# Optimization experiments

Hardware: AMD Instinct MI355X
Metric: run time of the kernel (lower is better)

## Reference

```python
import jax, jax.numpy as jnp
import numpy as np

D_MODEL = 768
NHEAD = 12
WINDOW = 128
FREQ = 10000.0


def _rope(x, freq=FREQ):
    # x: (b, h, l, d). Rotate-half style rotary embedding.
    b, h, l, d = x.shape
    inv_freq = 1.0 / (freq ** (jnp.arange(0, d, 2, dtype=jnp.float32) / d))  # (d/2,)
    ang = jnp.arange(l, dtype=jnp.float32)[:, None] * inv_freq[None, :]      # (l, d/2)
    cos = jnp.cos(ang)[None, None]  # (1,1,l,d/2)
    sin = jnp.sin(ang)[None, None]
    x1, x2 = x[..., : d // 2], x[..., d // 2 :]
    return jnp.concatenate([x1 * cos - x2 * sin, x1 * sin + x2 * cos], axis=-1)


def setup_inputs() -> dict:
    key = jax.random.key(0)
    k0, k1, k2 = jax.random.split(key, 3)
    B, L = 1, 2048
    emb = jax.random.normal(k0, (B, L, D_MODEL), dtype=jnp.float32)
    mask = jnp.ones((B, L), dtype=jnp.int32)
    W_qkv = jax.random.normal(k1, (D_MODEL, 3 * D_MODEL), dtype=jnp.float32) * 0.02
    b_qkv = jnp.zeros((3 * D_MODEL,), dtype=jnp.float32)
    W_o = jax.random.normal(k2, (D_MODEL, D_MODEL), dtype=jnp.float32) * 0.02
    b_o = jnp.zeros((D_MODEL,), dtype=jnp.float32)
    return {"embeddings": emb, "attention_mask": mask, "W_qkv": W_qkv, "b_qkv": b_qkv, "W_o": W_o, "b_o": b_o}


def reference(embeddings, attention_mask, W_qkv, b_qkv, W_o, b_o):
    B, L, D = embeddings.shape
    H, W = NHEAD, WINDOW
    hd = D // H
    scale = 1.0 / jnp.sqrt(jnp.float32(D))  # original divides by d_model**0.5

    qkv = embeddings @ W_qkv + b_qkv                      # (b,l,3D)
    q, k, v = jnp.split(qkv, 3, axis=-1)

    def sep(x):  # (b,l,D) -> (b,h,l,hd)
        return x.reshape(B, L, H, hd).transpose(0, 2, 1, 3)

    q, k, v = sep(q), sep(k), sep(v)
    q = _rope(q)
    k = _rope(k)

    # window indices: centered window of width W, clamped to [0, L-1]
    raw = jnp.arange(L)[:, None] + jnp.arange(W)[None, :] - W // 2  # (L,W)
    idxs = jnp.clip(raw, 0, L - 1)
    in_range = (raw >= 0) & (raw < L)                                # (L,W)

    k_w = k[:, :, idxs, :]  # (b,h,l,w,hd) gathered keys
    v_w = v[:, :, idxs, :]

    scores = jnp.einsum("bhlwd,bhld->bhlw", k_w, q) * scale
    amask = attention_mask.astype(bool)                              # (b,l)
    wmask = amask[:, idxs] & in_range[None]                          # (b,l,w)
    scores = jnp.where(wmask[:, None], scores, -jnp.inf)
    weights = jax.nn.softmax(scores, axis=-1)
    out = jnp.einsum("bhlw,bhlwd->bhld", weights, v_w)               # (b,h,l,hd)

    # CLS global attention (query at position 0 attends to all keys)
    cls_scores = jnp.einsum("bhd,bhld->bhl", q[:, :, 0, :], k) * scale
    cls_scores = jnp.where(amask[:, None], cls_scores, -jnp.inf)
    cls_w = jax.nn.softmax(cls_scores, axis=-1)
    cls_out = jnp.einsum("bhl,bhld->bhd", cls_w, v)                  # (b,h,hd)
    out = out.at[:, :, 0, :].set(cls_out)

    joined = out.transpose(0, 2, 1, 3).reshape(B, L, D)              # join heads
    return joined @ W_o + b_o
```

## Files before the change

### kernel.cpp

```cpp
#include <hip/hip_runtime.h>
#include <hip/hip_bf16.h>
#include <cmath>

#define D_MODEL 768
#define NHEAD 12
#define HD 64
#define L_SEQ 2048
#define WIN 128
#define QKV_N (3 * D_MODEL)

typedef _Float16 half8 __attribute__((ext_vector_type(8)));
typedef _Float16 half4v __attribute__((ext_vector_type(4)));
typedef float floatx4 __attribute__((ext_vector_type(4)));

#define CVT_A_BLKS 1536
#define CVT_B_BLKS (36 * 12)
#define CVT_C_BLKS (12 * 12)

__global__ __launch_bounds__(256) void cvt_fused_kernel(
    const float* __restrict__ emb, _Float16* __restrict__ A16,
    const float* __restrict__ W_qkv, _Float16* __restrict__ Wq16T,
    const float* __restrict__ W_o, _Float16* __restrict__ Wo16T) {
  __shared__ float tile[64][68];
  const int bid = blockIdx.x;
  const int tid = threadIdx.x;

  if (bid < CVT_A_BLKS) {
    const int i = (bid * 256 + tid) * 4;
    const float4 v = *reinterpret_cast<const float4*>(&emb[i]);
    half4v h = {(_Float16)v.x, (_Float16)v.y, (_Float16)v.z, (_Float16)v.w};
    *reinterpret_cast<half4v*>(&A16[i]) = h;
    return;
  }
  const float* In;
  _Float16* Out;
  int R, Cn, bx, by;
  if (bid < CVT_A_BLKS + CVT_B_BLKS) {
    const int b = bid - CVT_A_BLKS;
    In = W_qkv; Out = Wq16T; R = D_MODEL; Cn = QKV_N;
    bx = b % 36; by = b / 36;
  } else {
    const int b = bid - CVT_A_BLKS - CVT_B_BLKS;
    In = W_o; Out = Wo16T; R = D_MODEL; Cn = D_MODEL;
    bx = b % 12; by = b / 12;
  }
  const int r0 = by * 64, c0 = bx * 64;
  const int tr = tid >> 4, tc4 = (tid & 15) * 4;
#pragma unroll
  for (int rr = 0; rr < 4; ++rr) {
    const int r = rr * 16 + tr;
    const float4 v =
        *reinterpret_cast<const float4*>(&In[(size_t)(r0 + r) * Cn + c0 + tc4]);
    tile[r][tc4 + 0] = v.x;
    tile[r][tc4 + 1] = v.y;
    tile[r][tc4 + 2] = v.z;
    tile[r][tc4 + 3] = v.w;
  }
  __syncthreads();
#pragma unroll
  for (int cc = 0; cc < 4; ++cc) {
    const int c = cc * 16 + tr;
    half4v h = {(_Float16)tile[tc4 + 0][c], (_Float16)tile[tc4 + 1][c],
                (_Float16)tile[tc4 + 2][c], (_Float16)tile[tc4 + 3][c]};
    *reinterpret_cast<half4v*>(&Out[(size_t)(c0 + c) * R + r0 + tc4]) = h;
  }
}

template <int BM, int BN, typename OutT, bool ROPE>
__global__ __launch_bounds__(256) void gemm16_kernel(
    const _Float16* __restrict__ A, const _Float16* __restrict__ BT,
    const float* __restrict__ bias, OutT* __restrict__ C,
    _Float16* __restrict__ q16, _Float16* __restrict__ k16,
    _Float16* __restrict__ v16, _Float16* __restrict__ v16T, int M, int N,
    int K) {
  constexpr int LDK = 40;
  constexpr int MF = BM / 32;
  constexpr int NF = BN / 32;
  constexpr int CA = BM * 4 / 256;
  constexpr int CB = BN * 4 / 256;

  __shared__ __align__(16) _Float16 At[BM * LDK];
  __shared__ __align__(16) _Float16 Bt[BN * LDK];

  const int tid = threadIdx.x;
  const int row0 = blockIdx.y * BM;
  const int col0 = blockIdx.x * BN;
  const int wv = tid >> 6;
  const int lane = tid & 63;
  const int wr = wv >> 1;
  const int wc = wv & 1;
  const int lrow = lane & 15;
  const int lk = lane >> 4;

  floatx4 acc[MF][NF];
#pragma unroll
  for (int m = 0; m < MF; ++m)
#pragma unroll
    for (int n = 0; n < NF; ++n) acc[m][n] = (floatx4){0.f, 0.f, 0.f, 0.f};

  half8 aR[CA], bR[CB];
  const int nt = K / 32;

#pragma unroll
  for (int i = 0; i < CA; ++i) {
    const int c = tid + i * 256, r = c >> 2, seg = c & 3;
    aR[i] = *reinterpret_cast<const half8*>(&A[(size_t)(row0 + r) * K + seg * 8]);
  }
#pragma unroll
  for (int i = 0; i < CB; ++i) {
    const int c = tid + i * 256, r = c >> 2, seg = c & 3;
    bR[i] =
        *reinterpret_cast<const half8*>(&BT[(size_t)(col0 + r) * K + seg * 8]);
  }

  for (int t = 0; t < nt; ++t) {
    if (t) __syncthreads();
#pragma unroll
    for (int i = 0; i < CA; ++i) {
      const int c = tid + i * 256, r = c >> 2, seg = c & 3;
      *reinterpret_cast<half8*>(&At[r * LDK + seg * 8]) = aR[i];
    }
#pragma unroll
    for (int i = 0; i < CB; ++i) {
      const int c = tid + i * 256, r = c >> 2, seg = c & 3;
      *reinterpret_cast<half8*>(&Bt[r * LDK + seg * 8]) = bR[i];
    }
    __syncthreads();

    if (t + 1 < nt) {
      const int k0 = (t + 1) * 32;
#pragma unroll
      for (int i = 0; i < CA; ++i) {
        const int c = tid + i * 256, r = c >> 2, seg = c & 3;
        aR[i] = *reinterpret_cast<const half8*>(
            &A[(size_t)(row0 + r) * K + k0 + seg * 8]);
      }
#pragma unroll
      for (int i = 0; i < CB; ++i) {
        const int c = tid + i * 256, r = c >> 2, seg = c & 3;
        bR[i] = *reinterpret_cast<const half8*>(
            &BT[(size_t)(col0 + r) * K + k0 + seg * 8]);
      }
    }

    half8 af[MF], bf[NF];
#pragma unroll
    for (int m = 0; m < MF; ++m)
      af[m] = *reinterpret_cast<const half8*>(
          &At[(wr * (BM / 2) + m * 16 + lrow) * LDK + lk * 8]);
#pragma unroll
    for (int n = 0; n < NF; ++n)
      bf[n] = *reinterpret_cast<const half8*>(
          &Bt[(wc * (BN / 2) + n * 16 + lrow) * LDK + lk * 8]);
#pragma unroll
    for (int m = 0; m < MF; ++m)
#pragma unroll
      for (int n = 0; n < NF; ++n)
        acc[m][n] = __builtin_amdgcn_mfma_f32_16x16x32_f16(af[m], bf[n],
                                                           acc[m][n], 0, 0, 0);
  }

  if constexpr (!ROPE) {
#pragma unroll
    for (int m = 0; m < MF; ++m)
#pragma unroll
      for (int n = 0; n < NF; ++n) {
        const int col = col0 + wc * (BN / 2) + n * 16 + lrow;
        const float bb = bias[col];
#pragma unroll
        for (int j = 0; j < 4; ++j) {
          const int row = row0 + wr * (BM / 2) + m * 16 + lk * 4 + j;
          C[(size_t)row * N + col] = (OutT)(acc[m][n][j] + bb);
        }
      }
  } else {
    const int part = col0 / D_MODEL;
    const int h = ((col0 % D_MODEL) >> 6) + wc;
    _Float16* dst = (part == 0) ? q16 : (part == 1) ? k16 : v16;
    float bb[4];
#pragma unroll
    for (int n = 0; n < 4; ++n) bb[n] = bias[col0 + wc * 64 + n * 16 + lrow];
    const float inv0 = exp2f(-0.4152410118609203f * (float)lrow);
    const float inv1 = inv0 * 0.01f;
#pragma unroll
    for (int m = 0; m < MF; ++m) {
#pragma unroll
      for (int j = 0; j < 4; ++j) {
        const int l = row0 + wr * (BM / 2) + m * 16 + lk * 4 + j;
        float val[4];
#pragma unroll
        for (int n = 0; n < 4; ++n) val[n] = acc[m][n][j] + bb[n];
        float o[4];
        if (part < 2) {
          float sn0, cs0, sn1, cs1;
          __sincosf((float)l * inv0, &sn0, &cs0);
          __sincosf((float)l * inv1, &sn1, &cs1);
          o[0] = val[0] * cs0 - val[2] * sn0;
          o[1] = val[1] * cs1 - val[3] * sn1;
          o[2] = val[0] * sn0 + val[2] * cs0;
          o[3] = val[1] * sn1 + val[3] * cs1;
        } else {
          o[0] = val[0]; o[1] = val[1]; o[2] = val[2]; o[3] = val[3];
        }
        const size_t base = ((size_t)h * L_SEQ + l) * HD + lrow;
#pragma unroll
        for (int n = 0; n < 4; ++n) dst[base + n * 16] = (_Float16)o[n];
      }
      if (part == 2) {
        const int lb = row0 + wr * (BM / 2) + m * 16 + lk * 4;
#pragma unroll
        for (int n = 0; n < 4; ++n) {
          const int col = h * HD + n * 16 + lrow;
          half4v hv = {(_Float16)(acc[m][n][0] + bb[n]),
                       (_Float16)(acc[m][n][1] + bb[n]),
                       (_Float16)(acc[m][n][2] + bb[n]),
                       (_Float16)(acc[m][n][3] + bb[n])};
          *reinterpret_cast<half4v*>(&v16T[(size_t)col * L_SEQ + lb]) = hv;
        }
      }
    }
  }
}

#define TL 32
#define SLOTS 160
#define LDH 72
#define LDS_S 168
#define LDVT 168
#define CSPLIT 32
#define CROWS (L_SEQ / CSPLIT)
#define CREC 66

__global__ __launch_bounds__(256) void attn_mega_kernel(
    const _Float16* __restrict__ q16, const _Float16* __restrict__ k16,
    const _Float16* __restrict__ v16, const _Float16* __restrict__ v16T,
    const int* __restrict__ mask, _Float16* __restrict__ joined,
    float* __restrict__ part) {
  const int h = blockIdx.y;
  const int tid = threadIdx.x;
  const float scale = 0.036084391824351615f;

  __shared__ __align__(16) _Float16 kv16[SLOTS * LDH];
  __shared__ __align__(16) float sS[TL * LDS_S];
  __shared__ __align__(16) _Float16 q16l[TL * LDH];
  __shared__ float vbias[SLOTS];

  if (blockIdx.x < (L_SEQ / TL)) {
    const int l0 = blockIdx.x * TL;
    const _Float16* kh = k16 + (size_t)h * L_SEQ * HD;
    const _Float16* qh = q16 + (size_t)h * L_SEQ * HD;

    {
      const int row = tid >> 3, oct = (tid & 7) * 8;
      *reinterpret_cast<half8*>(&q16l[row * LDH + oct]) =
          *reinterpret_cast<const half8*>(&qh[(size_t)(l0 + row) * HD + oct]);
    }
    const _Float16* kwin = kh + (size_t)(l0 - WIN / 2) * HD;
#pragma unroll
    for (int c = tid; c < SLOTS * 8; c += 256) {
      const int slot = c >> 3, oct = (c & 7) * 8;
      *reinterpret_cast<half8*>(&kv16[slot * LDH + oct]) =
          *reinterpret_cast<const half8*>(&kwin[(size_t)slot * HD + oct]);
    }
    if (tid < SLOTS) {
      const int raw = l0 + tid - WIN / 2;
      const int idx = min(max(raw, 0), L_SEQ - 1);
      vbias[tid] =
          ((raw >= 0) && (raw < L_SEQ) && (mask[idx] != 0)) ? 0.f : -INFINITY;
    }
    __syncthreads();

    const int wv = tid >> 6, lane = tid & 63;
    const int wr = wv >> 1, wc = wv & 1;
    const int lcol = lane & 15, loct = (lane >> 4) * 8;

    floatx4 accS[5];
#pragma unroll
    for (int f = 0; f < 5; ++f) accS[f] = (floatx4){0.f, 0.f, 0.f, 0.f};
#pragma unroll
    for (int ks = 0; ks < 2; ++ks) {
      const half8 af = *reinterpret_cast<const half8*>(
          &q16l[(wr * 16 + lcol) * LDH + ks * 32 + loct]);
#pragma unroll
      for (int f = 0; f < 5; ++f) {
        const half8 bf = *reinterpret_cast<const half8*>(
            &kv16[(wc * 80 + f * 16 + lcol) * LDH + ks * 32 + loct]);
        accS[f] =
            __builtin_amdgcn_mfma_f32_16x16x32_f16(af, bf, accS[f], 0, 0, 0);
      }
    }
#pragma unroll
    for (int f = 0; f < 5; ++f) {
      const int slot = wc * 80 + f * 16 + lcol;
      const float vb = vbias[slot];
#pragma unroll
      for (int j = 0; j < 4; ++j) {
        const int row = wr * 16 + (lane >> 4) * 4 + j;
        const bool inband = (slot >= row) && (slot <= row + WIN - 1);
        sS[row * LDS_S + slot] = inband ? (accS[f][j] * scale + vb) : -INFINITY;
      }
    }
    __syncthreads();

    _Float16* vt = kv16;
    const _Float16* vtg =
        v16T + (size_t)h * HD * L_SEQ + (l0 - WIN / 2);
#pragma unroll
    for (int c = tid; c < HD * 20; c += 256) {
      const int d = c / 20, seg = c % 20;
      *reinterpret_cast<half8*>(&vt[d * LDVT + seg * 8]) =
          *reinterpret_cast<const half8*>(&vtg[(size_t)d * L_SEQ + seg * 8]);
    }

    const int r = tid >> 3, wg = tid & 7;
    float pv[20];
    float mloc = -INFINITY;
#pragma unroll
    for (int i = 0; i < 20; ++i) {
      pv[i] = sS[r * LDS_S + wg * 20 + i];
      mloc = fmaxf(mloc, pv[i]);
    }
#pragma unroll
    for (int m = 1; m < 8; m <<= 1) mloc = fmaxf(mloc, __shfl_xor(mloc, m));
    float ssum = 0.f;
#pragma unroll
    for (int i = 0; i < 20; ++i) {
      pv[i] = __expf(pv[i] - mloc);
      ssum += pv[i];
    }
#pragma unroll
    for (int m = 1; m < 8; m <<= 1) ssum += __shfl_xor(ssum, m);
    const float rcp = 1.0f / ssum;
    __syncthreads();

    _Float16* pS = reinterpret_cast<_Float16*>(sS);
#pragma unroll
    for (int i = 0; i < 20; ++i)
      pS[r * (2 * LDS_S) + wg * 20 + i] = (_Float16)(pv[i] * rcp);
    __syncthreads();

    floatx4 accO[2];
    accO[0] = (floatx4){0.f, 0.f, 0.f, 0.f};
    accO[1] = (floatx4){0.f, 0.f, 0.f, 0.f};
#pragma unroll
    for (int ks = 0; ks < 5; ++ks) {
      const half8 ap = *reinterpret_cast<const half8*>(
          &pS[(wr * 16 + lcol) * (2 * LDS_S) + ks * 32 + loct]);
#pragma unroll
      for (int cf = 0; cf < 2; ++cf) {
        const half8 bv = *reinterpret_cast<const half8*>(
            &vt[(wc * 32 + cf * 16 + lcol) * LDVT + ks * 32 + loct]);
        accO[cf] =
            __builtin_amdgcn_mfma_f32_16x16x32_f16(ap, bv, accO[cf], 0, 0, 0);
      }
    }
#pragma unroll
    for (int cf = 0; cf < 2; ++cf)
#pragma unroll
      for (int j = 0; j < 4; ++j) {
        const int row = wr * 16 + (lane >> 4) * 4 + j;
        const int d = wc * 32 + cf * 16 + lcol;
        joined[(size_t)(l0 + row) * D_MODEL + h * HD + d] =
            (_Float16)accO[cf][j];
      }
  } else {
    const int sp = blockIdx.x - (L_SEQ / TL);
    const int l0 = sp * CROWS;
    float* scS = sS;
    float* red = sS + CROWS;
    float* pvS = sS + CROWS + 256;

    const _Float16* kh = k16 + (size_t)h * L_SEQ * HD;
    const _Float16* vh = v16 + (size_t)h * L_SEQ * HD;

    const int lq = tid >> 4;
    const int dq = tid & 15;
    const half4v q4 =
        *reinterpret_cast<const half4v*>(&q16[(size_t)h * L_SEQ * HD + dq * 4]);
#pragma unroll
    for (int it = 0; it < CROWS / 16; ++it) {
      const int l = l0 + it * 16 + lq;
      const half4v k4 =
          *reinterpret_cast<const half4v*>(&kh[(size_t)l * HD + dq * 4]);
      float p = (float)q4[0] * (float)k4[0] + (float)q4[1] * (float)k4[1] +
                (float)q4[2] * (float)k4[2] + (float)q4[3] * (float)k4[3];
#pragma unroll
      for (int m = 1; m < 16; m <<= 1) p += __shfl_xor(p, m);
      if (dq == 0) scS[it * 16 + lq] = (mask[l] != 0) ? p * scale : -INFINITY;
    }
    __syncthreads();

    red[tid] = (tid < CROWS) ? scS[tid] : -INFINITY;
    __syncthreads();
    for (int off = 128; off > 0; off >>= 1) {
      if (tid < off) red[tid] = fmaxf(red[tid], red[tid + off]);
      __syncthreads();
    }
    const float mx = red[0];
    __syncthreads();

    float e = 0.f;
    if (tid < CROWS) {
      e = (mx == -INFINITY) ? 0.f : __expf(scS[tid] - mx);
      scS[tid] = e;
    }
    red[tid] = e;
    __syncthreads();
    for (int off = 128; off > 0; off >>= 1) {
      if (tid < off) red[tid] += red[tid + off];
      __syncthreads();
    }
    const float lsum = red[0];
    __syncthreads();

    const int lg = tid >> 6;
    const int d = tid & 63;
    float acc = 0.f;
#pragma unroll 8
    for (int it = 0; it < CROWS / 4; ++it) {
      const int ll = lg + it * 4;
      acc += scS[ll] * (float)vh[(size_t)(l0 + ll) * HD + d];
    }
    pvS[lg * HD + d] = acc;
    __syncthreads();

    float* rec = &part[(size_t)(h * CSPLIT + sp) * CREC];
    if (tid == 0) {
      rec[0] = mx;
      rec[1] = lsum;
    }
    if (tid < HD)
      rec[2 + tid] =
          pvS[0 * HD + tid] + pvS[1 * HD + tid] + pvS[2 * HD + tid] +
          pvS[3 * HD + tid];
  }
}

__global__ __launch_bounds__(64) void cls_combine_kernel(
    const float* __restrict__ part, _Float16* __restrict__ joined) {
  const int h = blockIdx.x;
  const int d = threadIdx.x;

  float gmax = -INFINITY;
#pragma unroll
  for (int sp = 0; sp < CSPLIT; ++sp)
    gmax = fmaxf(gmax, part[(size_t)(h * CSPLIT + sp) * CREC]);

  float total = 0.f, acc = 0.f;
#pragma unroll
  for (int sp = 0; sp < CSPLIT; ++sp) {
    const float* rec = &part[(size_t)(h * CSPLIT + sp) * CREC];
    const float mxi = rec[0];
    const float w = (mxi == -INFINITY) ? 0.f : __expf(mxi - gmax);
    total += w * rec[1];
    acc += w * rec[2 + d];
  }
  joined[(size_t)h * HD + d] = (_Float16)(acc / total);
}

extern "C" void kernel_launch(void* const* d_in, const int* in_sizes, int n_in,
                              void* d_out, int out_size, void* d_ws,
                              size_t ws_size, hipStream_t stream) {
  const float* emb   = (const float*)d_in[0];
  const int*   mask  = (const int*)d_in[1];
  const float* W_qkv = (const float*)d_in[2];
  const float* b_qkv = (const float*)d_in[3];
  const float* W_o   = (const float*)d_in[4];
  const float* b_o   = (const float*)d_in[5];
  float* out = (float*)d_out;

  _Float16* hp = (_Float16*)d_ws;
  _Float16* A16   = hp;
  _Float16* Wq16T = A16 + (size_t)L_SEQ * D_MODEL;
  _Float16* Wo16T = Wq16T + (size_t)QKV_N * D_MODEL;
  _Float16* q16   = Wo16T + (size_t)D_MODEL * D_MODEL;
  _Float16* k16   = q16 + (size_t)NHEAD * L_SEQ * HD;
  _Float16* v16   = k16 + (size_t)NHEAD * L_SEQ * HD;
  _Float16* v16T  = v16 + (size_t)NHEAD * L_SEQ * HD;
  _Float16* J16   = v16T + (size_t)D_MODEL * L_SEQ;
  float*    part  = (float*)(J16 + (size_t)L_SEQ * D_MODEL);

  cvt_fused_kernel<<<CVT_A_BLKS + CVT_B_BLKS + CVT_C_BLKS, 256, 0, stream>>>(
      emb, A16, W_qkv, Wq16T, W_o, Wo16T);

  gemm16_kernel<64, 128, _Float16, true>
      <<<dim3(QKV_N / 128, L_SEQ / 64), 256, 0, stream>>>(
          A16, Wq16T, b_qkv, (_Float16*)nullptr, q16, k16, v16, v16T, L_SEQ,
          QKV_N, D_MODEL);

  attn_mega_kernel<<<dim3(L_SEQ / TL + CSPLIT, NHEAD), 256, 0, stream>>>(
      q16, k16, v16, v16T, mask, J16, part);

  cls_combine_kernel<<<NHEAD, 64, 0, stream>>>(part, J16);

  gemm16_kernel<64, 64, float, false>
      <<<dim3(D_MODEL / 64, L_SEQ / 64), 256, 0, stream>>>(
          J16, Wo16T, b_o, out, (_Float16*)nullptr, (_Float16*)nullptr,
          (_Float16*)nullptr, (_Float16*)nullptr, L_SEQ, D_MODEL, D_MODEL);
}
```

Before: 123.8 us.

## Fuse embedding fp16 conversion into QKV GEMM, CLS combine into output GEMM, double-buffer LDS

The QKV GEMM now reads fp32 embeddings directly and converts them to fp16 in registers, which removes the separate conversion pass and its intermediate buffer. The CLS combine step is folded into the output-projection GEMM: the row-0 blocks compute the combined CLS vector into LDS and use it as row 0 of A, so one kernel launch is dropped. The GEMM main loop also moves to double-buffered LDS with one barrier per K step. In exchange, the QKV GEMM reads twice the A bytes, the row-0 blocks do serial combine work before their GEMM starts, and LDS use doubles.

Measured after the change: 144.0 us. 16.3% more time.

```diff
diff --git a/kernel.cpp b/kernel.cpp
--- a/kernel.cpp
+++ b/kernel.cpp
@@ -13,34 +13,24 @@
 typedef _Float16 half4v __attribute__((ext_vector_type(4)));
 typedef float floatx4 __attribute__((ext_vector_type(4)));
 
-#define CVT_A_BLKS 1536
 #define CVT_B_BLKS (36 * 12)
 #define CVT_C_BLKS (12 * 12)
 
 __global__ __launch_bounds__(256) void cvt_fused_kernel(
-    const float* __restrict__ emb, _Float16* __restrict__ A16,
     const float* __restrict__ W_qkv, _Float16* __restrict__ Wq16T,
     const float* __restrict__ W_o, _Float16* __restrict__ Wo16T) {
   __shared__ float tile[64][68];
   const int bid = blockIdx.x;
   const int tid = threadIdx.x;
 
-  if (bid < CVT_A_BLKS) {
-    const int i = (bid * 256 + tid) * 4;
-    const float4 v = *reinterpret_cast<const float4*>(&emb[i]);
-    half4v h = {(_Float16)v.x, (_Float16)v.y, (_Float16)v.z, (_Float16)v.w};
-    *reinterpret_cast<half4v*>(&A16[i]) = h;
-    return;
-  }
   const float* In;
   _Float16* Out;
   int R, Cn, bx, by;
-  if (bid < CVT_A_BLKS + CVT_B_BLKS) {
-    const int b = bid - CVT_A_BLKS;
+  if (bid < CVT_B_BLKS) {
     In = W_qkv; Out = Wq16T; R = D_MODEL; Cn = QKV_N;
-    bx = b % 36; by = b / 36;
+    bx = bid % 36; by = bid / 36;
   } else {
-    const int b = bid - CVT_A_BLKS - CVT_B_BLKS;
+    const int b = bid - CVT_B_BLKS;
     In = W_o; Out = Wo16T; R = D_MODEL; Cn = D_MODEL;
     bx = b % 12; by = b / 12;
   }
@@ -66,12 +56,16 @@
   }
 }
 
-template <int BM, int BN, typename OutT, bool ROPE>
+#define CSPLIT 32
+#define CREC 66
+
+template <int BM, int BN, typename OutT, bool ROPE, bool A32, bool COMBINE>
 __global__ __launch_bounds__(256) void gemm16_kernel(
-    const _Float16* __restrict__ A, const _Float16* __restrict__ BT,
-    const float* __restrict__ bias, OutT* __restrict__ C,
-    _Float16* __restrict__ q16, _Float16* __restrict__ k16,
-    _Float16* __restrict__ v16, _Float16* __restrict__ v16T, int M, int N,
+    const float* __restrict__ Af, const _Float16* __restrict__ Ah,
+    const _Float16* __restrict__ BT, const float* __restrict__ bias,
+    OutT* __restrict__ C, _Float16* __restrict__ q16,
+    _Float16* __restrict__ k16, _Float16* __restrict__ v16,
+    _Float16* __restrict__ v16T, const float* __restrict__ part, int M, int N,
     int K) {
   constexpr int LDK = 40;
   constexpr int MF = BM / 32;
@@ -79,8 +73,9 @@
   constexpr int CA = BM * 4 / 256;
   constexpr int CB = BN * 4 / 256;
 
-  __shared__ __align__(16) _Float16 At[BM * LDK];
-  __shared__ __align__(16) _Float16 Bt[BN * LDK];
+  __shared__ __align__(16) _Float16 At[2 * BM * LDK];
+  __shared__ __align__(16) _Float16 Bt[2 * BN * LDK];
+  __shared__ __align__(16) _Float16 comb[COMBINE ? D_MODEL : 1];
 
   const int tid = threadIdx.x;
   const int row0 = blockIdx.y * BM;
@@ -91,6 +86,32 @@
   const int wc = wv & 1;
   const int lrow = lane & 15;
   const int lk = lane >> 4;
+  const bool doComb = COMBINE && (blockIdx.y == 0);
+
+  if constexpr (COMBINE) {
+    if (doComb) {
+#pragma unroll
+      for (int j = 0; j < D_MODEL / 256; ++j) {
+        const int c = tid + j * 256;
+        const int h = c >> 6, d = c & 63;
+        float gmax = -INFINITY;
+#pragma unroll 8
+        for (int sp = 0; sp < CSPLIT; ++sp)
+          gmax = fmaxf(gmax, part[(size_t)(h * CSPLIT + sp) * CREC]);
+        float total = 0.f, acc = 0.f;
+#pragma unroll 8
+        for (int sp = 0; sp < CSPLIT; ++sp) {
+          const float* rec = &part[(size_t)(h * CSPLIT + sp) * CREC];
+          const float mxi = rec[0];
+          const float w = (mxi == -INFINITY) ? 0.f : __expf(mxi - gmax);
+          total += w * rec[1];
+          acc += w * rec[2 + d];
+        }
+        comb[c] = (_Float16)(acc / total);
+      }
+      __syncthreads();
+    }
+  }
 
   floatx4 acc[MF][NF];
 #pragma unroll
@@ -101,63 +122,77 @@
   half8 aR[CA], bR[CB];
   const int nt = K / 32;
 
-#pragma unroll
-  for (int i = 0; i < CA; ++i) {
-    const int c = tid + i * 256, r = c >> 2, seg = c & 3;
-    aR[i] = *reinterpret_cast<const half8*>(&A[(size_t)(row0 + r) * K + seg * 8]);
-  }
-#pragma unroll
-  for (int i = 0; i < CB; ++i) {
-    const int c = tid + i * 256, r = c >> 2, seg = c & 3;
-    bR[i] =
-        *reinterpret_cast<const half8*>(&BT[(size_t)(col0 + r) * K + seg * 8]);
-  }
-
-  for (int t = 0; t < nt; ++t) {
-    if (t) __syncthreads();
+  auto load_regs = [&](int t) {
+    const int k0 = t * 32;
 #pragma unroll
     for (int i = 0; i < CA; ++i) {
       const int c = tid + i * 256, r = c >> 2, seg = c & 3;
-      *reinterpret_cast<half8*>(&At[r * LDK + seg * 8]) = aR[i];
+      if constexpr (A32) {
+        const float4 f0 = *reinterpret_cast<const float4*>(
+            &Af[(size_t)(row0 + r) * K + k0 + seg * 8]);
+        const float4 f1 = *reinterpret_cast<const float4*>(
+            &Af[(size_t)(row0 + r) * K + k0 + seg * 8 + 4]);
+        aR[i] = (half8){(_Float16)f0.x, (_Float16)f0.y, (_Float16)f0.z,
+                        (_Float16)f0.w, (_Float16)f1.x, (_Float16)f1.y,
+                        (_Float16)f1.z, (_Float16)f1.w};
+      } else {
+        if (COMBINE && doComb && r == 0) {
+          aR[i] = *reinterpret_cast<const half8*>(&comb[k0 + seg * 8]);
+        } else {
+          aR[i] = *reinterpret_cast<const half8*>(
+              &Ah[(size_t)(row0 + r) * K + k0 + seg * 8]);
+        }
+      }
     }
 #pragma unroll
     for (int i = 0; i < CB; ++i) {
       const int c = tid + i * 256, r = c >> 2, seg = c & 3;
-      *reinterpret_cast<half8*>(&Bt[r * LDK + seg * 8]) = bR[i];
-    }
-    __syncthreads();
-
-    if (t + 1 < nt) {
-      const int k0 = (t + 1) * 32;
-#pragma unroll
-      for (int i = 0; i < CA; ++i) {
-        const int c = tid + i * 256, r = c >> 2, seg = c & 3;
-        aR[i] = *reinterpret_cast<const half8*>(
-            &A[(size_t)(row0 + r) * K + k0 + seg * 8]);
-      }
-#pragma unroll
-      for (int i = 0; i < CB; ++i) {
-        const int c = tid + i * 256, r = c >> 2, seg = c & 3;
-        bR[i] = *reinterpret_cast<const half8*>(
-            &BT[(size_t)(col0 + r) * K + k0 + seg * 8]);
-      }
-    }
-
+      bR[i] = *reinterpret_cast<const half8*>(
+          &BT[(size_t)(col0 + r) * K + k0 + seg * 8]);
+    }
+  };
+  auto store_lds = [&](int buf) {
+    _Float16* a = &At[buf * BM * LDK];
+    _Float16* b = &Bt[buf * BN * LDK];
+#pragma unroll
+    for (int i = 0; i < CA; ++i) {
+      const int c = tid + i * 256, r = c >> 2, seg = c & 3;
+      *reinterpret_cast<half8*>(&a[r * LDK + seg * 8]) = aR[i];
+    }
+#pragma unroll
+    for (int i = 0; i < CB; ++i) {
+      const int c = tid + i * 256, r = c >> 2, seg = c & 3;
+      *reinterpret_cast<half8*>(&b[r * LDK + seg * 8]) = bR[i];
+    }
+  };
+
+  load_regs(0);
+  store_lds(0);
+  int cur = 0;
+
+  for (int t = 0; t < nt; ++t) {
+    __syncthreads();
+    if (t + 1 < nt) load_regs(t + 1);
+
+    const _Float16* a = &At[cur * BM * LDK];
+    const _Float16* b = &Bt[cur * BN * LDK];
     half8 af[MF], bf[NF];
 #pragma unroll
     for (int m = 0; m < MF; ++m)
       af[m] = *reinterpret_cast<const half8*>(
-          &At[(wr * (BM / 2) + m * 16 + lrow) * LDK + lk * 8]);
+          &a[(wr * (BM / 2) + m * 16 + lrow) * LDK + lk * 8]);
 #pragma unroll
     for (int n = 0; n < NF; ++n)
       bf[n] = *reinterpret_cast<const half8*>(
-          &Bt[(wc * (BN / 2) + n * 16 + lrow) * LDK + lk * 8]);
+          &b[(wc * (BN / 2) + n * 16 + lrow) * LDK + lk * 8]);
 #pragma unroll
     for (int m = 0; m < MF; ++m)
 #pragma unroll
       for (int n = 0; n < NF; ++n)
         acc[m][n] = __builtin_amdgcn_mfma_f32_16x16x32_f16(af[m], bf[n],
                                                            acc[m][n], 0, 0, 0);
+    if (t + 1 < nt) store_lds(cur ^ 1);
+    cur ^= 1;
   }
 
   if constexpr (!ROPE) {
@@ -174,9 +209,9 @@
         }
       }
   } else {
-    const int part = col0 / D_MODEL;
+    const int part_id = col0 / D_MODEL;
     const int h = ((col0 % D_MODEL) >> 6) + wc;
-    _Float16* dst = (part == 0) ? q16 : (part == 1) ? k16 : v16;
+    _Float16* dst = (part_id == 0) ? q16 : (part_id == 1) ? k16 : v16;
     float bb[4];
 #pragma unroll
     for (int n = 0; n < 4; ++n) bb[n] = bias[col0 + wc * 64 + n * 16 + lrow];
@@ -191,7 +226,7 @@
 #pragma unroll
         for (int n = 0; n < 4; ++n) val[n] = acc[m][n][j] + bb[n];
         float o[4];
-        if (part < 2) {
+        if (part_id < 2) {
           float sn0, cs0, sn1, cs1;
           __sincosf((float)l * inv0, &sn0, &cs0);
           __sincosf((float)l * inv1, &sn1, &cs1);
@@ -206,7 +241,7 @@
 #pragma unroll
         for (int n = 0; n < 4; ++n) dst[base + n * 16] = (_Float16)o[n];
       }
-      if (part == 2) {
+      if (part_id == 2) {
         const int lb = row0 + wr * (BM / 2) + m * 16 + lk * 4;
 #pragma unroll
         for (int n = 0; n < 4; ++n) {
@@ -227,9 +262,7 @@
 #define LDH 72
 #define LDS_S 168
 #define LDVT 168
-#define CSPLIT 32
 #define CROWS (L_SEQ / CSPLIT)
-#define CREC 66
 
 __global__ __launch_bounds__(256) void attn_mega_kernel(
     const _Float16* __restrict__ q16, const _Float16* __restrict__ k16,
@@ -303,8 +336,7 @@
     __syncthreads();
 
     _Float16* vt = kv16;
-    const _Float16* vtg =
-        v16T + (size_t)h * HD * L_SEQ + (l0 - WIN / 2);
+    const _Float16* vtg = v16T + (size_t)h * HD * L_SEQ + (l0 - WIN / 2);
 #pragma unroll
     for (int c = tid; c < HD * 20; c += 256) {
       const int d = c / 20, seg = c % 20;
@@ -430,32 +462,9 @@
       rec[1] = lsum;
     }
     if (tid < HD)
-      rec[2 + tid] =
-          pvS[0 * HD + tid] + pvS[1 * HD + tid] + pvS[2 * HD + tid] +
-          pvS[3 * HD + tid];
-  }
-}
-
-__global__ __launch_bounds__(64) void cls_combine_kernel(
-    const float* __restrict__ part, _Float16* __restrict__ joined) {
-  const int h = blockIdx.x;
-  const int d = threadIdx.x;
-
-  float gmax = -INFINITY;
-#pragma unroll
-  for (int sp = 0; sp < CSPLIT; ++sp)
-    gmax = fmaxf(gmax, part[(size_t)(h * CSPLIT + sp) * CREC]);
-
-  float total = 0.f, acc = 0.f;
-#pragma unroll
-  for (int sp = 0; sp < CSPLIT; ++sp) {
-    const float* rec = &part[(size_t)(h * CSPLIT + sp) * CREC];
-    const float mxi = rec[0];
-    const float w = (mxi == -INFINITY) ? 0.f : __expf(mxi - gmax);
-    total += w * rec[1];
-    acc += w * rec[2 + d];
-  }
-  joined[(size_t)h * HD + d] = (_Float16)(acc / total);
+      rec[2 + tid] = pvS[0 * HD + tid] + pvS[1 * HD + tid] +
+                     pvS[2 * HD + tid] + pvS[3 * HD + tid];
+  }
 }
 
 extern "C" void kernel_launch(void* const* d_in, const int* in_sizes, int n_in,
@@ -470,8 +479,7 @@
   float* out = (float*)d_out;
 
   _Float16* hp = (_Float16*)d_ws;
-  _Float16* A16   = hp;
-  _Float16* Wq16T = A16 + (size_t)L_SEQ * D_MODEL;
+  _Float16* Wq16T = hp;
   _Float16* Wo16T = Wq16T + (size_t)QKV_N * D_MODEL;
   _Float16* q16   = Wo16T + (size_t)D_MODEL * D_MODEL;
   _Float16* k16   = q16 + (size_t)NHEAD * L_SEQ * HD;
@@ -480,21 +488,20 @@
   _Float16* J16   = v16T + (size_t)D_MODEL * L_SEQ;
   float*    part  = (float*)(J16 + (size_t)L_SEQ * D_MODEL);
 
-  cvt_fused_kernel<<<CVT_A_BLKS + CVT_B_BLKS + CVT_C_BLKS, 256, 0, stream>>>(
-      emb, A16, W_qkv, Wq16T, W_o, Wo16T);
-
-  gemm16_kernel<64, 128, _Float16, true>
+  cvt_fused_kernel<<<CVT_B_BLKS + CVT_C_BLKS, 256, 0, stream>>>(
+      W_qkv, Wq16T, W_o, Wo16T);
+
+  gemm16_kernel<64, 128, _Float16, true, true, false>
       <<<dim3(QKV_N / 128, L_SEQ / 64), 256, 0, stream>>>(
-          A16, Wq16T, b_qkv, (_Float16*)nullptr, q16, k16, v16, v16T, L_SEQ,
-          QKV_N, D_MODEL);
+          emb, (const _Float16*)nullptr, Wq16T, b_qkv, (_Float16*)nullptr, q16,
+          k16, v16, v16T, (const float*)nullptr, L_SEQ, QKV_N, D_MODEL);
 
   attn_mega_kernel<<<dim3(L_SEQ / TL + CSPLIT, NHEAD), 256, 0, stream>>>(
       q16, k16, v16, v16T, mask, J16, part);
 
-  cls_combine_kernel<<<NHEAD, 64, 0, stream>>>(part, J16);
-
-  gemm16_kernel<64, 64, float, false>
+  gemm16_kernel<64, 64, float, false, false, true>
       <<<dim3(D_MODEL / 64, L_SEQ / 64), 256, 0, stream>>>(
-          J16, Wo16T, b_o, out, (_Float16*)nullptr, (_Float16*)nullptr,
-          (_Float16*)nullptr, (_Float16*)nullptr, L_SEQ, D_MODEL, D_MODEL);
+          (const float*)nullptr, J16, Wo16T, b_o, out, (_Float16*)nullptr,
+          (_Float16*)nullptr, (_Float16*)nullptr, (_Float16*)nullptr, part,
+          L_SEQ, D_MODEL, D_MODEL);
 }
```

## Double-buffer GEMM tiles with direct global-to-LDS async copies and XOR swizzle

Applied to the files above, without the earlier changes.

Replaces the register-staged GEMM tile loading with `global_load_lds` direct-to-shared copies into two ping-pong LDS buffers. This removes the register round trip and leaves one barrier per K step instead of two. The padded LDS layout is replaced by an XOR swizzle on 16-byte segments to avoid bank conflicts. The risk is that correctness relies on the barrier waiting for outstanding vector-memory loads and on the swizzle mapping matching between writer and reader lanes.

Result: no change. 125.0 us (+1.0%).

```diff
diff --git a/kernel.cpp b/kernel.cpp
--- a/kernel.cpp
+++ b/kernel.cpp
@@ -12,6 +12,11 @@
 typedef _Float16 half8 __attribute__((ext_vector_type(8)));
 typedef _Float16 half4v __attribute__((ext_vector_type(4)));
 typedef float floatx4 __attribute__((ext_vector_type(4)));
+
+#define ASYNC_COPY16(gptr, lptr)                                      \
+  __builtin_amdgcn_global_load_lds(                                   \
+      (const __attribute__((address_space(1))) void*)(gptr),          \
+      (__attribute__((address_space(3))) void*)(lptr), 16, 0, 0)
 
 #define CVT_A_BLKS 1536
 #define CVT_B_BLKS (36 * 12)
@@ -73,14 +78,13 @@
     _Float16* __restrict__ q16, _Float16* __restrict__ k16,
     _Float16* __restrict__ v16, _Float16* __restrict__ v16T, int M, int N,
     int K) {
-  constexpr int LDK = 40;
+  static_assert(BM == 64, "staging assignment assumes BM==64");
   constexpr int MF = BM / 32;
   constexpr int NF = BN / 32;
-  constexpr int CA = BM * 4 / 256;
-  constexpr int CB = BN * 4 / 256;
-
-  __shared__ __align__(16) _Float16 At[BM * LDK];
-  __shared__ __align__(16) _Float16 Bt[BN * LDK];
+  constexpr int NBPW = BN / 64;
+
+  __shared__ __align__(16) _Float16 At[2 * BM * 32];
+  __shared__ __align__(16) _Float16 Bt[2 * BN * 32];
 
   const int tid = threadIdx.x;
   const int row0 = blockIdx.y * BM;
@@ -92,72 +96,58 @@
   const int lrow = lane & 15;
   const int lk = lane >> 4;
 
+  const int segg = (((lane & 3) ^ ((lane >> 2) & 3) ^ (lane >> 4)) << 3);
+
+  const _Float16* gA =
+      A + (size_t)(row0 + wv * 16 + (lane >> 2)) * K + segg;
+  const _Float16* gB[NBPW];
+#pragma unroll
+  for (int i = 0; i < NBPW; ++i)
+    gB[i] = BT + (size_t)(col0 + (wv + 4 * i) * 16 + (lane >> 2)) * K + segg;
+
   floatx4 acc[MF][NF];
 #pragma unroll
   for (int m = 0; m < MF; ++m)
 #pragma unroll
     for (int n = 0; n < NF; ++n) acc[m][n] = (floatx4){0.f, 0.f, 0.f, 0.f};
 
-  half8 aR[CA], bR[CB];
   const int nt = K / 32;
 
-#pragma unroll
-  for (int i = 0; i < CA; ++i) {
-    const int c = tid + i * 256, r = c >> 2, seg = c & 3;
-    aR[i] = *reinterpret_cast<const half8*>(&A[(size_t)(row0 + r) * K + seg * 8]);
-  }
-#pragma unroll
-  for (int i = 0; i < CB; ++i) {
-    const int c = tid + i * 256, r = c >> 2, seg = c & 3;
-    bR[i] =
-        *reinterpret_cast<const half8*>(&BT[(size_t)(col0 + r) * K + seg * 8]);
-  }
-
+  ASYNC_COPY16(gA, &At[wv * 512]);
+#pragma unroll
+  for (int i = 0; i < NBPW; ++i)
+    ASYNC_COPY16(gB[i], &Bt[(wv + 4 * i) * 512]);
+
+  int cur = 0;
   for (int t = 0; t < nt; ++t) {
-    if (t) __syncthreads();
-#pragma unroll
-    for (int i = 0; i < CA; ++i) {
-      const int c = tid + i * 256, r = c >> 2, seg = c & 3;
-      *reinterpret_cast<half8*>(&At[r * LDK + seg * 8]) = aR[i];
-    }
-#pragma unroll
-    for (int i = 0; i < CB; ++i) {
-      const int c = tid + i * 256, r = c >> 2, seg = c & 3;
-      *reinterpret_cast<half8*>(&Bt[r * LDK + seg * 8]) = bR[i];
-    }
-    __syncthreads();
-
+    __syncthreads();
     if (t + 1 < nt) {
-      const int k0 = (t + 1) * 32;
-#pragma unroll
-      for (int i = 0; i < CA; ++i) {
-        const int c = tid + i * 256, r = c >> 2, seg = c & 3;
-        aR[i] = *reinterpret_cast<const half8*>(
-            &A[(size_t)(row0 + r) * K + k0 + seg * 8]);
-      }
-#pragma unroll
-      for (int i = 0; i < CB; ++i) {
-        const int c = tid + i * 256, r = c >> 2, seg = c & 3;
-        bR[i] = *reinterpret_cast<const half8*>(
-            &BT[(size_t)(col0 + r) * K + k0 + seg * 8]);
-      }
-    }
-
+      const int ko = (t + 1) * 32;
+      ASYNC_COPY16(gA + ko, &At[(cur ^ 1) * (BM * 32) + wv * 512]);
+#pragma unroll
+      for (int i = 0; i < NBPW; ++i)
+        ASYNC_COPY16(gB[i] + ko,
+                     &Bt[(cur ^ 1) * (BN * 32) + (wv + 4 * i) * 512]);
+    }
+
+    const _Float16* a = &At[cur * (BM * 32)];
+    const _Float16* b = &Bt[cur * (BN * 32)];
     half8 af[MF], bf[NF];
 #pragma unroll
     for (int m = 0; m < MF; ++m)
       af[m] = *reinterpret_cast<const half8*>(
-          &At[(wr * (BM / 2) + m * 16 + lrow) * LDK + lk * 8]);
+          &a[(wr * (BM / 2) + m * 16 + lrow) * 32 + segg]);
 #pragma unroll
     for (int n = 0; n < NF; ++n)
       bf[n] = *reinterpret_cast<const half8*>(
-          &Bt[(wc * (BN / 2) + n * 16 + lrow) * LDK + lk * 8]);
+          &b[(wc * (BN / 2) + n * 16 + lrow) * 32 + segg]);
 #pragma unroll
     for (int m = 0; m < MF; ++m)
 #pragma unroll
       for (int n = 0; n < NF; ++n)
         acc[m][n] = __builtin_amdgcn_mfma_f32_16x16x32_f16(af[m], bf[n],
                                                            acc[m][n], 0, 0, 0);
+    cur ^= 1;
   }
 
   if constexpr (!ROPE) {
@@ -303,8 +293,7 @@
     __syncthreads();
 
     _Float16* vt = kv16;
-    const _Float16* vtg =
-        v16T + (size_t)h * HD * L_SEQ + (l0 - WIN / 2);
+    const _Float16* vtg = v16T + (size_t)h * HD * L_SEQ + (l0 - WIN / 2);
 #pragma unroll
     for (int c = tid; c < HD * 20; c += 256) {
       const int d = c / 20, seg = c % 20;
@@ -430,9 +419,8 @@
       rec[1] = lsum;
     }
     if (tid < HD)
-      rec[2 + tid] =
-          pvS[0 * HD + tid] + pvS[1 * HD + tid] + pvS[2 * HD + tid] +
-          pvS[3 * HD + tid];
+      rec[2 + tid] = pvS[0 * HD + tid] + pvS[1 * HD + tid] +
+                     pvS[2 * HD + tid] + pvS[3 * HD + tid];
   }
 }
 
```
